# Performance work log

Hardware: AMD Instinct MI355X
Metric: run time of the kernel (lower is better)

The kernel has to match this reference:

```python
import jax, jax.numpy as jnp
import numpy as np

B, K, U = 4096, 512, 3
P, LIFT, HID, NSUB = 5, 32, 128, 10
RATE_LO, RATE_HI = 0.01, 3.0
BASAL_LO, BASAL_HI = 0.0, 0.3


def _xavier(key, shape):
    fan_in, fan_out = shape[1], shape[0]
    lim = np.sqrt(6.0 / (fan_in + fan_out))
    return jax.random.uniform(key, shape, jnp.float32, -lim, lim)


def setup_inputs() -> dict:
    key = jax.random.key(0)
    ks = jax.random.split(key, 10)
    return {
        "y0": jax.random.uniform(ks[0], (B, P), jnp.float32),
        "u_seq": jax.random.uniform(ks[1], (B, K, U), jnp.float32),
        "dt_seq": jax.random.uniform(ks[2], (B, K), jnp.float32),
        # lift: Linear(in_u+P -> LIFT)
        "Wl": _xavier(ks[3], (LIFT, U + P)),
        "bl": jnp.zeros((LIFT,), jnp.float32),
        # GRU (single layer): weight_ih (3H, LIFT), weight_hh (3H, H)
        "W_ih": _xavier(ks[4], (3 * HID, LIFT)),
        "b_ih": jnp.zeros((3 * HID,), jnp.float32),
        "W_hh": _xavier(ks[5], (3 * HID, HID)),
        "b_hh": jnp.zeros((3 * HID,), jnp.float32),
        # head: Linear(H -> 13)
        "Wh": _xavier(ks[6], (13, HID)),
        "bh": jnp.zeros((13,), jnp.float32),
        # bolus-to-state jump matrix (in_u, P)
        "u_to_y_jump": 0.1 * jax.random.uniform(ks[7], (U, P), jnp.float32),
    }


def _rhs(y, theta):
    # y: (B,5) [A,D,G,J,M]; theta: (B,13) [kf1..4, kr1..4, kj1..5]
    A, D, G, J, M = (y[:, i] for i in range(5))
    kf1, kf2, kf3, kf4, kr1, kr2, kr3, kr4, kj1, kj2, kj3, kj4, kj5 = (
        theta[:, i] for i in range(13))
    dA = -kf1 * A + kr1 * D + kj1
    dD = kf1 * A - kr1 * D - kf2 * D + kr2 * G + kj2
    dG = kf2 * D - kr2 * G - kf3 * G + kr3 * J + kj3
    dJ = kf3 * G - kr3 * J - kf4 * J + kr4 * M + kj4
    dM = kf4 * J - kr4 * M + kj5
    return jnp.stack([dA, dD, dG, dJ, dM], axis=-1)


def _rk4(y, h, theta):
    # h: (B,1) substep size
    k1 = _rhs(y, theta)
    k2 = _rhs(y + 0.5 * h * k1, theta)
    k3 = _rhs(y + 0.5 * h * k2, theta)
    k4 = _rhs(y + h * k3, theta)
    return jnp.maximum(y + h / 6.0 * (k1 + 2.0 * k2 + 2.0 * k3 + k4), 0.0)


def reference(y0, u_seq, dt_seq, Wl, bl, W_ih, b_ih, W_hh, b_hh, Wh, bh, u_to_y_jump):
    Bb = y0.shape[0]
    hid = W_hh.shape[1]

    def step(carry, inp):
        y_prev, hst = carry
        u_k, dt_k = inp  # (B,U), (B,)
        feat = jnp.concatenate([u_k, jax.lax.stop_gradient(y_prev)], axis=-1)
        x = jax.nn.silu(feat @ Wl.T + bl)
        # PyTorch GRUCell math
        gx = x @ W_ih.T + b_ih
        gh = hst @ W_hh.T + b_hh
        gxr, gxz, gxn = jnp.split(gx, 3, axis=-1)
        ghr, ghz, ghn = jnp.split(gh, 3, axis=-1)
        r = jax.nn.sigmoid(gxr + ghr)
        zg = jax.nn.sigmoid(gxz + ghz)
        n = jnp.tanh(gxn + r * ghn)
        h_new = (1.0 - zg) * n + zg * hst
        raw = h_new @ Wh.T + bh
        rates = RATE_LO + (RATE_HI - RATE_LO) * jax.nn.sigmoid(raw[:, 0:8])
        basal = BASAL_LO + (BASAL_HI - BASAL_LO) * jax.nn.sigmoid(raw[:, 8:13])
        theta = jnp.concatenate([rates, basal], axis=-1)
        y = y_prev + u_k @ u_to_y_jump
        hsub = (dt_k / float(NSUB))[:, None]
        for _ in range(NSUB):
            y = _rk4(y, hsub, theta)
        return (y, h_new), (y, theta)

    y_init = y0 + 0.01
    h0 = jnp.zeros((Bb, hid), dtype=y0.dtype)
    # scan over time: (K,B,...)
    _, (ys, thetas) = jax.lax.scan(
        step, (y_init, h0), (u_seq.transpose(1, 0, 2), dt_seq.T))
    y_out = ys.transpose(1, 0, 2)        # (B,K,P)
    theta_out = thetas.transpose(1, 0, 2)  # (B,K,13)
    return y_out, theta_out
```

## Files before the change

kernel.cpp:

```cpp
#include <hip/hip_runtime.h>
#include <cstdint>
#include <cstddef>


#define KTOT 512
#define BB   16

typedef _Float16 half8 __attribute__((ext_vector_type(8)));
typedef float    f32x4 __attribute__((ext_vector_type(4)));

struct __align__(16) Smem {
  _Float16 hf16[BB][136];
  float Wlt[8][32];
  float bl[32];
  float brz[256];
  float bnx[128];
  float bnh[128];
  float bhv[16];
  float theta[BB][14];
  float yst[BB][8];
  float ust[2][BB][4];
  float dtst[2][BB];
};

__device__ __forceinline__ float sigm(float x)     { return 1.f / (1.f + __expf(-x)); }
__device__ __forceinline__ float tanhfast(float x) { return 1.f - 2.f / (1.f + __expf(2.f * x)); }

template<int CTRL>
__device__ __forceinline__ float dppf(float x) {
  return __int_as_float(__builtin_amdgcn_mov_dpp(__float_as_int(x), CTRL, 0xf, 0xf, true));
}
#define QP_PLUS  0x39
#define QP_MINUS 0x93
#define QB0 0x00
#define QB1 0x55
#define QB2 0xAA
#define QB3 0xFF

#define MATMUL(Yr, Y4r, Xr, X4r, ALPHA) do {                                  \
  float xm_[5], xp_[5];                                                       \
  _Pragma("unroll")                                                           \
  for (int j_ = 0; j_ < 5; j_++) {                                            \
    xm_[j_] = dppf<QP_MINUS>(Xr[j_]);                                         \
    xp_[j_] = dppf<QP_PLUS >(Xr[j_]);                                         \
  }                                                                           \
  _Pragma("unroll")                                                           \
  for (int j_ = 0; j_ < 5; j_++) {                                            \
    const float ac_ = Zl*xm_[j_] + Zd*Xr[j_] + Zu*xp_[j_] + Zu4*X4r[j_];      \
    const float a4_ = Z43*Xr[j_] + Z44*X4r[j_];                               \
    Yr[j_]  = ((j_ == s_) ? 1.f : 0.f) + (ALPHA)*ac_;                         \
    Y4r[j_] = ((j_ == 4 ) ? 1.f : 0.f) + (ALPHA)*a4_;                         \
  } } while (0)

__global__ __launch_bounds__(256, 1) void rnn_scan_kernel(
    const float* __restrict__ y0,    const float* __restrict__ u_seq,
    const float* __restrict__ dt_sq, const float* __restrict__ Wl,
    const float* __restrict__ bl,    const float* __restrict__ W_ih,
    const float* __restrict__ b_ih,  const float* __restrict__ W_hh,
    const float* __restrict__ b_hh,  const float* __restrict__ Wh,
    const float* __restrict__ bh,    const float* __restrict__ jmp,
    float* __restrict__ y_out, float* __restrict__ th_out)
{
  __shared__ Smem sm;
  const int t   = threadIdx.x;
  const int w   = t >> 6;
  const int l   = t & 63;
  const int n16 = l & 15;
  const int q   = l >> 4;
  const int B0  = blockIdx.x * BB;

  for (int i = t; i < 32*8; i += 256) { const int oo = i >> 3, c = i & 7;
    sm.Wlt[c][oo] = Wl[i]; }
  if (t < 32)  sm.bl[t] = bl[t];
  sm.brz[t] = b_ih[t] + b_hh[t];
  if (t < 128) { sm.bnx[t] = b_ih[256+t]; sm.bnh[t] = b_hh[256+t]; }
  if (t < 16)  sm.bhv[t] = (t < 13) ? bh[t] : 0.f;
  if (t < 128) { const int b = t >> 3, i = t & 7;
    sm.yst[b][i] = (i < 5) ? (y0[(size_t)(B0+b)*5 + i] + 0.01f) : 0.f; }
  if (t < 48) { const int b = t/3, c = t - b*3;
    sm.ust[0][b][c] = u_seq[((size_t)(B0+b)*KTOT + 0)*3 + c]; }
  if (t >= 48 && t < 64) sm.dtst[0][t-48] = dt_sq[(size_t)(B0+(t-48))*KTOT + 0];

  half8 whf[4];
  #pragma unroll
  for (int ks = 0; ks < 4; ks++)
    #pragma unroll
    for (int i = 0; i < 8; i++) {
      const int kk = ks*32 + q*8 + i;
      whf[ks][i] = (n16 < 13) ? (_Float16)Wh[n16*128 + kk] : (_Float16)0.f;
    }

  half8 wihR[2], wihZ[2], wihN[2], whhR[2][4], whhZ[2][4], whhN[2][4];
  #pragma unroll
  for (int p = 0; p < 2; p++) {
    const int jR = (2*w + p)*16 + n16;
    const int jZ = jR + 128, jN = jR + 256;
    #pragma unroll
    for (int i = 0; i < 8; i++) {
      const int kk = q*8 + i;
      wihR[p][i] = (_Float16)W_ih[jR*32 + kk];
      wihZ[p][i] = (_Float16)W_ih[jZ*32 + kk];
      wihN[p][i] = (_Float16)W_ih[jN*32 + kk];
    }
    #pragma unroll
    for (int ks = 0; ks < 4; ks++)
      #pragma unroll
      for (int i = 0; i < 8; i++) {
        const int kk = ks*32 + q*8 + i;
        whhR[p][ks][i] = (_Float16)W_hh[jR*128 + kk];
        whhZ[p][ks][i] = (_Float16)W_hh[jZ*128 + kk];
        whhN[p][ks][i] = (_Float16)W_hh[jN*128 + kk];
      }
  }

  float hreg[2][4];
  #pragma unroll
  for (int p = 0; p < 2; p++)
    #pragma unroll
    for (int rg = 0; rg < 4; rg++) hreg[p][rg] = 0.f;
  half8 hfrag[4];
  #pragma unroll
  for (int ks = 0; ks < 4; ks++)
    #pragma unroll
    for (int i = 0; i < 8; i++) hfrag[ks][i] = (_Float16)0.f;

  const int s_ = l & 3, b4 = l >> 2;
  const float jr0 = jmp[0*5 + s_], jr1 = jmp[1*5 + s_], jr2 = jmp[2*5 + s_];
  const float j40 = (s_==3) ? jmp[4]  : 0.f;
  const float j41 = (s_==3) ? jmp[9]  : 0.f;
  const float j42 = (s_==3) ? jmp[14] : 0.f;

  const int yb = t/5, yi = t - yb*5;
  float* yo_base = y_out + ((size_t)(B0 + (yb & 15))*KTOT)*5 + yi;
  const int ts = (t >= 48) ? (t - 48) : 0;
  const int tb = ts/13, tn = ts - tb*13;
  float* th_base = th_out + ((size_t)(B0 + tb)*KTOT)*13 + tn;
  const int upb = l/3, upc = l - upb*3;

  __syncthreads();

  const f32x4 zero4 = {0.f, 0.f, 0.f, 0.f};

  #pragma unroll 1
  for (int k = 0; k < KTOT; k++) {
    const int buf  = k & 1;
    const int nbuf = (k + 1) & 1;
    const int kp   = (k + 1 < KTOT) ? (k + 1) : (KTOT - 1);

    float pref_u = 0.f, pref_dt = 0.f;
    if (w == 1 && l < 48)
      pref_u = u_seq[((size_t)(B0 + upb)*KTOT + kp)*3 + upc];
    if (w == 2 && l < 16)
      pref_dt = dt_sq[(size_t)(B0 + l)*KTOT + kp];
    if (k > 0) {
      if (t < 80)  yo_base[(size_t)(k-1)*5]  = sm.yst[yb][yi];
      if (t >= 48) th_base[(size_t)(k-1)*13] = sm.theta[tb][tn];
    }
    const float u0 = sm.ust[buf][n16][0], u1 = sm.ust[buf][n16][1], u2 = sm.ust[buf][n16][2];
    const float ya = sm.yst[n16][0], yB = sm.yst[n16][1], yc = sm.yst[n16][2],
                yd = sm.yst[n16][3], ye = sm.yst[n16][4];
    half8 xf;
    #pragma unroll
    for (int i = 0; i < 8; i++) {
      const int oo = q*8 + i;
      const float a = sm.bl[oo]
        + u0*sm.Wlt[0][oo] + u1*sm.Wlt[1][oo] + u2*sm.Wlt[2][oo]
        + ya*sm.Wlt[3][oo] + yB*sm.Wlt[4][oo] + yc*sm.Wlt[5][oo]
        + yd*sm.Wlt[6][oo] + ye*sm.Wlt[7][oo];
      xf[i] = (_Float16)(a * sigm(a));
    }
    f32x4 accR[2], accZ[2], accXN[2], accHN[2];
    #pragma unroll
    for (int p = 0; p < 2; p++) {
      accR[p]  = __builtin_amdgcn_mfma_f32_16x16x32_f16(xf, wihR[p], zero4, 0,0,0);
      accZ[p]  = __builtin_amdgcn_mfma_f32_16x16x32_f16(xf, wihZ[p], zero4, 0,0,0);
      accXN[p] = __builtin_amdgcn_mfma_f32_16x16x32_f16(xf, wihN[p], zero4, 0,0,0);
      accHN[p] = zero4;
      #pragma unroll
      for (int ks = 0; ks < 4; ks++) {
        accR[p]  = __builtin_amdgcn_mfma_f32_16x16x32_f16(hfrag[ks], whhR[p][ks], accR[p], 0,0,0);
        accZ[p]  = __builtin_amdgcn_mfma_f32_16x16x32_f16(hfrag[ks], whhZ[p][ks], accZ[p], 0,0,0);
        accHN[p] = __builtin_amdgcn_mfma_f32_16x16x32_f16(hfrag[ks], whhN[p][ks], accHN[p], 0,0,0);
      }
    }
    #pragma unroll
    for (int p = 0; p < 2; p++) {
      const int jl = 32*w + 16*p + n16;
      const float br = sm.brz[jl], bz = sm.brz[128 + jl];
      const float bx = sm.bnx[jl], bn = sm.bnh[jl];
      #pragma unroll
      for (int rg = 0; rg < 4; rg++) {
        const float r  = sigm(accR[p][rg] + br);
        const float z  = sigm(accZ[p][rg] + bz);
        const float nn = tanhfast(accXN[p][rg] + bx + r*(accHN[p][rg] + bn));
        const float ho = hreg[p][rg];
        const float hn = nn + z*(ho - nn);
        hreg[p][rg] = hn;
        sm.hf16[q*4 + rg][jl] = (_Float16)hn;
      }
    }
    if (w == 1 && l < 48) sm.ust[nbuf][upb][upc] = pref_u;
    if (w == 2 && l < 16) sm.dtst[nbuf][l] = pref_dt;
    __syncthreads();

    #pragma unroll
    for (int ks = 0; ks < 4; ks++)
      hfrag[ks] = *(const half8*)&sm.hf16[n16][ks*32 + q*8];

    if (w == 0) {
      f32x4 accH = zero4;
      #pragma unroll
      for (int ks = 0; ks < 4; ks++)
        accH = __builtin_amdgcn_mfma_f32_16x16x32_f16(hfrag[ks], whf[ks], accH, 0,0,0);
      const float bb_ = sm.bhv[n16];
      #pragma unroll
      for (int rg = 0; rg < 4; rg++) {
        const float sg  = sigm(accH[rg] + bb_);
        const float thv = (n16 < 8) ? (0.01f + 2.99f*sg) : (0.3f*sg);
        if (n16 < 13) sm.theta[q*4 + rg][n16] = thv;
      }
      const float* th = sm.theta[b4];
      const float dt = sm.dtst[buf][b4];
      const float h  = dt * 0.1f;
      const float thm = th[s_ ? (s_ - 1) : 0];
      const float Zl  = s_ ? h*thm : 0.f;
      const float krs = s_ ? th[3 + s_] : 0.f;
      const float Zd  = -h*(th[s_] + krs);
      const float Zur = h*th[4 + s_];
      const float Zu  = (s_ < 3) ? Zur : 0.f;
      const float Zu4 = (s_ == 3) ? Zur : 0.f;
      const float Z43 = h*th[3];
      const float Z44 = -h*th[7];
      const float c0 = th[8], c1 = th[9], c2 = th[10], c3 = th[11], c4 = th[12];
      float Xa[5], Xa4[5], Xb[5], Xb4[5];
      #pragma unroll
      for (int j = 0; j < 5; j++) {
        const float zr = (j == s_) ? Zd : ((j == s_ + 1) ? Zur : ((j + 1 == s_) ? Zl : 0.f));
        Xa[j] = ((j == s_) ? 1.f : 0.f) + 0.25f*zr;
      }
      Xa4[0] = 0.f; Xa4[1] = 0.f; Xa4[2] = 0.f;
      Xa4[3] = 0.25f*Z43; Xa4[4] = 1.f + 0.25f*Z44;
      MATMUL(Xb, Xb4, Xa, Xa4, (1.f/3.f));
      MATMUL(Xa, Xa4, Xb, Xb4, 0.5f);
      const float bv  = h*(Xa[0]*c0 + Xa[1]*c1 + Xa[2]*c2 + Xa[3]*c3 + Xa[4]*c4);
      const float bv4 = h*(Xa4[0]*c0 + Xa4[1]*c1 + Xa4[2]*c2 + Xa4[3]*c3 + Xa4[4]*c4);
      MATMUL(Xb, Xb4, Xa, Xa4, 1.f);
      const float uu0 = sm.ust[buf][b4][0], uu1 = sm.ust[buf][b4][1], uu2 = sm.ust[buf][b4][2];
      float y  = sm.yst[b4][s_] + uu0*jr0 + uu1*jr1 + uu2*jr2;
      float y4 = sm.yst[b4][4]  + uu0*j40 + uu1*j41 + uu2*j42;
      #pragma unroll
      for (int ss = 0; ss < 10; ss++) {
        const float v0 = dppf<QB0>(y), v1 = dppf<QB1>(y),
                    v2 = dppf<QB2>(y), v3 = dppf<QB3>(y);
        const float v4 = dppf<QB3>(y4);
        const float yn  = fmaxf(bv  + Xb[0]*v0 + Xb[1]*v1 + Xb[2]*v2 + Xb[3]*v3 + Xb[4]*v4, 0.f);
        const float y4n = fmaxf(bv4 + Xb4[0]*v0 + Xb4[1]*v1 + Xb4[2]*v2 + Xb4[3]*v3 + Xb4[4]*v4, 0.f);
        y = yn; y4 = y4n;
      }
      sm.yst[b4][s_] = y;
      if (s_ == 3) sm.yst[b4][4] = y4;
    }
    __syncthreads();
  }

  if (t < 80)  yo_base[(size_t)(KTOT-1)*5]  = sm.yst[yb][yi];
  if (t >= 48) th_base[(size_t)(KTOT-1)*13] = sm.theta[tb][tn];
}

extern "C" void kernel_launch(void* const* d_in, const int* in_sizes, int n_in,
                              void* d_out, int out_size, void* d_ws, size_t ws_size,
                              hipStream_t stream) {
  const float* y0     = (const float*)d_in[0];
  const float* u_seq  = (const float*)d_in[1];
  const float* dt_sq  = (const float*)d_in[2];
  const float* Wl     = (const float*)d_in[3];
  const float* bl     = (const float*)d_in[4];
  const float* W_ih   = (const float*)d_in[5];
  const float* b_ih   = (const float*)d_in[6];
  const float* W_hh   = (const float*)d_in[7];
  const float* b_hh   = (const float*)d_in[8];
  const float* Wh     = (const float*)d_in[9];
  const float* bh     = (const float*)d_in[10];
  const float* jmp    = (const float*)d_in[11];
  float* y_out  = (float*)d_out;
  float* th_out = y_out + (size_t)4096 * KTOT * 5;
  rnn_scan_kernel<<<256, 256, 0, stream>>>(
      y0, u_seq, dt_sq, Wl, bl, W_ih, b_ih, W_hh, b_hh, Wh, bh, jmp, y_out, th_out);
}
```

Baseline: 1.687 ms.

## Split GRU gates across 8 waves and precompute hidden matmul ahead of lift

```diff
diff --git a/kernel.cpp b/kernel.cpp
--- a/kernel.cpp
+++ b/kernel.cpp
@@ -11,8 +11,7 @@
 
 struct __align__(16) Smem {
   _Float16 hf16[BB][136];
-  float Wlt[8][32];
-  float bl[32];
+  _Float16 xls[BB][32];
   float brz[256];
   float bnx[128];
   float bnh[128];
@@ -52,7 +51,7 @@
     Y4r[j_] = ((j_ == 4 ) ? 1.f : 0.f) + (ALPHA)*a4_;                         \
   } } while (0)
 
-__global__ __launch_bounds__(256, 1) void rnn_scan_kernel(
+__global__ __launch_bounds__(512, 2) void rnn_scan_kernel(
     const float* __restrict__ y0,    const float* __restrict__ u_seq,
     const float* __restrict__ dt_sq, const float* __restrict__ Wl,
     const float* __restrict__ bl,    const float* __restrict__ W_ih,
@@ -69,17 +68,21 @@
   const int q   = l >> 4;
   const int B0  = blockIdx.x * BB;
 
-  for (int i = t; i < 32*8; i += 256) { const int oo = i >> 3, c = i & 7;
-    sm.Wlt[c][oo] = Wl[i]; }
-  if (t < 32)  sm.bl[t] = bl[t];
-  sm.brz[t] = b_ih[t] + b_hh[t];
+  if (t < 256) sm.brz[t] = b_ih[t] + b_hh[t];
   if (t < 128) { sm.bnx[t] = b_ih[256+t]; sm.bnh[t] = b_hh[256+t]; }
   if (t < 16)  sm.bhv[t] = (t < 13) ? bh[t] : 0.f;
-  if (t < 128) { const int b = t >> 3, i = t & 7;
+  if (t >= 256 && t < 384) { const int b = (t-256) >> 3, i = (t-256) & 7;
     sm.yst[b][i] = (i < 5) ? (y0[(size_t)(B0+b)*5 + i] + 0.01f) : 0.f; }
-  if (t < 48) { const int b = t/3, c = t - b*3;
+  if (t >= 384 && t < 432) { const int b = (t-384)/3, c = (t-384) - ((t-384)/3)*3;
     sm.ust[0][b][c] = u_seq[((size_t)(B0+b)*KTOT + 0)*3 + c]; }
-  if (t >= 48 && t < 64) sm.dtst[0][t-48] = dt_sq[(size_t)(B0+(t-48))*KTOT + 0];
+  if (t >= 432 && t < 448) sm.dtst[0][t-432] = dt_sq[(size_t)(B0+(t-432))*KTOT + 0];
+
+  const int lb = t >> 5;
+  const int lo = t & 31;
+  float wlc[8];
+  #pragma unroll
+  for (int c = 0; c < 8; c++) wlc[c] = Wl[lo*8 + c];
+  const float blv = bl[lo];
 
   half8 whf[4];
   #pragma unroll
@@ -90,39 +93,29 @@
       whf[ks][i] = (n16 < 13) ? (_Float16)Wh[n16*128 + kk] : (_Float16)0.f;
     }
 
-  half8 wihR[2], wihZ[2], wihN[2], whhR[2][4], whhZ[2][4], whhN[2][4];
-  #pragma unroll
-  for (int p = 0; p < 2; p++) {
-    const int jR = (2*w + p)*16 + n16;
-    const int jZ = jR + 128, jN = jR + 256;
+  const int jR = w*16 + n16;
+  const int jZ = jR + 128, jN = jR + 256;
+  half8 wihR, wihZ, wihN, whhR[4], whhZ[4], whhN[4];
+  #pragma unroll
+  for (int i = 0; i < 8; i++) {
+    const int kk = q*8 + i;
+    wihR[i] = (_Float16)W_ih[jR*32 + kk];
+    wihZ[i] = (_Float16)W_ih[jZ*32 + kk];
+    wihN[i] = (_Float16)W_ih[jN*32 + kk];
+  }
+  #pragma unroll
+  for (int ks = 0; ks < 4; ks++)
     #pragma unroll
     for (int i = 0; i < 8; i++) {
-      const int kk = q*8 + i;
-      wihR[p][i] = (_Float16)W_ih[jR*32 + kk];
-      wihZ[p][i] = (_Float16)W_ih[jZ*32 + kk];
-      wihN[p][i] = (_Float16)W_ih[jN*32 + kk];
-    }
-    #pragma unroll
-    for (int ks = 0; ks < 4; ks++)
-      #pragma unroll
-      for (int i = 0; i < 8; i++) {
-        const int kk = ks*32 + q*8 + i;
-        whhR[p][ks][i] = (_Float16)W_hh[jR*128 + kk];
-        whhZ[p][ks][i] = (_Float16)W_hh[jZ*128 + kk];
-        whhN[p][ks][i] = (_Float16)W_hh[jN*128 + kk];
-      }
-  }
-
-  float hreg[2][4];
-  #pragma unroll
-  for (int p = 0; p < 2; p++)
-    #pragma unroll
-    for (int rg = 0; rg < 4; rg++) hreg[p][rg] = 0.f;
-  half8 hfrag[4];
-  #pragma unroll
-  for (int ks = 0; ks < 4; ks++)
-    #pragma unroll
-    for (int i = 0; i < 8; i++) hfrag[ks][i] = (_Float16)0.f;
+      const int kk = ks*32 + q*8 + i;
+      whhR[ks][i] = (_Float16)W_hh[jR*128 + kk];
+      whhZ[ks][i] = (_Float16)W_hh[jZ*128 + kk];
+      whhN[ks][i] = (_Float16)W_hh[jN*128 + kk];
+    }
+
+  float hreg[4] = {0.f, 0.f, 0.f, 0.f};
+  const f32x4 zero4 = {0.f, 0.f, 0.f, 0.f};
+  f32x4 accPreR = zero4, accPreZ = zero4, accPreN = zero4;
 
   const int s_ = l & 3, b4 = l >> 2;
   const float jr0 = jmp[0*5 + s_], jr1 = jmp[1*5 + s_], jr2 = jmp[2*5 + s_];
@@ -130,16 +123,20 @@
   const float j41 = (s_==3) ? jmp[9]  : 0.f;
   const float j42 = (s_==3) ? jmp[14] : 0.f;
 
-  const int yb = t/5, yi = t - yb*5;
+  const int yb = t/5, yi = t - (t/5)*5;
   float* yo_base = y_out + ((size_t)(B0 + (yb & 15))*KTOT)*5 + yi;
-  const int ts = (t >= 48) ? (t - 48) : 0;
-  const int tb = ts/13, tn = ts - tb*13;
-  float* th_base = th_out + ((size_t)(B0 + tb)*KTOT)*13 + tn;
-  const int upb = l/3, upc = l - upb*3;
+  const int ts = (t >= 80) ? (t - 80) : 0;
+  const int tb = ts/13, tn = ts - (ts/13)*13;
+  float* th_base = th_out + ((size_t)(B0 + (tb & 15))*KTOT)*13 + tn;
+  const int upb = l/3, upc = l - (l/3)*3;
 
   __syncthreads();
 
-  const f32x4 zero4 = {0.f, 0.f, 0.f, 0.f};
+  const float br  = sm.brz[jR];
+  const float bz  = sm.brz[128 + jR];
+  const float bx  = sm.bnx[jR];
+  const float bn  = sm.bnh[jR];
+  const float bb_ = sm.bhv[n16];
 
   #pragma unroll 1
   for (int k = 0; k < KTOT; k++) {
@@ -147,72 +144,64 @@
     const int nbuf = (k + 1) & 1;
     const int kp   = (k + 1 < KTOT) ? (k + 1) : (KTOT - 1);
 
+    {
+      const f32x4 uu = *(const f32x4*)&sm.ust[buf][lb][0];
+      const f32x4 ya = *(const f32x4*)&sm.yst[lb][0];
+      const f32x4 yc = *(const f32x4*)&sm.yst[lb][4];
+      const float a = blv
+        + uu[0]*wlc[0] + uu[1]*wlc[1] + uu[2]*wlc[2]
+        + ya[0]*wlc[3] + ya[1]*wlc[4] + ya[2]*wlc[5] + ya[3]*wlc[6]
+        + yc[0]*wlc[7];
+      sm.xls[lb][lo] = (_Float16)(a * sigm(a));
+    }
+    __syncthreads();
+
+    if (k > 0) {
+      if (t < 80)        yo_base[(size_t)(k-1)*5]  = sm.yst[yb][yi];
+      else if (t < 288)  th_base[(size_t)(k-1)*13] = sm.theta[tb][tn];
+    }
+    {
+      const half8 xf = *(const half8*)&sm.xls[n16][q*8];
+      const f32x4 accR  = __builtin_amdgcn_mfma_f32_16x16x32_f16(xf, wihR, accPreR, 0,0,0);
+      const f32x4 accZ  = __builtin_amdgcn_mfma_f32_16x16x32_f16(xf, wihZ, accPreZ, 0,0,0);
+      const f32x4 accXN = __builtin_amdgcn_mfma_f32_16x16x32_f16(xf, wihN, zero4,   0,0,0);
+      #pragma unroll
+      for (int rg = 0; rg < 4; rg++) {
+        const float r  = sigm(accR[rg] + br);
+        const float z  = sigm(accZ[rg] + bz);
+        const float nn = tanhfast(accXN[rg] + bx + r*(accPreN[rg] + bn));
+        const float ho = hreg[rg];
+        const float hn = nn + z*(ho - nn);
+        hreg[rg] = hn;
+        sm.hf16[q*4 + rg][jR] = (_Float16)hn;
+      }
+    }
+    __syncthreads();
+
     float pref_u = 0.f, pref_dt = 0.f;
     if (w == 1 && l < 48)
       pref_u = u_seq[((size_t)(B0 + upb)*KTOT + kp)*3 + upc];
     if (w == 2 && l < 16)
       pref_dt = dt_sq[(size_t)(B0 + l)*KTOT + kp];
-    if (k > 0) {
-      if (t < 80)  yo_base[(size_t)(k-1)*5]  = sm.yst[yb][yi];
-      if (t >= 48) th_base[(size_t)(k-1)*13] = sm.theta[tb][tn];
-    }
-    const float u0 = sm.ust[buf][n16][0], u1 = sm.ust[buf][n16][1], u2 = sm.ust[buf][n16][2];
-    const float ya = sm.yst[n16][0], yB = sm.yst[n16][1], yc = sm.yst[n16][2],
-                yd = sm.yst[n16][3], ye = sm.yst[n16][4];
-    half8 xf;
-    #pragma unroll
-    for (int i = 0; i < 8; i++) {
-      const int oo = q*8 + i;
-      const float a = sm.bl[oo]
-        + u0*sm.Wlt[0][oo] + u1*sm.Wlt[1][oo] + u2*sm.Wlt[2][oo]
-        + ya*sm.Wlt[3][oo] + yB*sm.Wlt[4][oo] + yc*sm.Wlt[5][oo]
-        + yd*sm.Wlt[6][oo] + ye*sm.Wlt[7][oo];
-      xf[i] = (_Float16)(a * sigm(a));
-    }
-    f32x4 accR[2], accZ[2], accXN[2], accHN[2];
-    #pragma unroll
-    for (int p = 0; p < 2; p++) {
-      accR[p]  = __builtin_amdgcn_mfma_f32_16x16x32_f16(xf, wihR[p], zero4, 0,0,0);
-      accZ[p]  = __builtin_amdgcn_mfma_f32_16x16x32_f16(xf, wihZ[p], zero4, 0,0,0);
-      accXN[p] = __builtin_amdgcn_mfma_f32_16x16x32_f16(xf, wihN[p], zero4, 0,0,0);
-      accHN[p] = zero4;
-      #pragma unroll
-      for (int ks = 0; ks < 4; ks++) {
-        accR[p]  = __builtin_amdgcn_mfma_f32_16x16x32_f16(hfrag[ks], whhR[p][ks], accR[p], 0,0,0);
-        accZ[p]  = __builtin_amdgcn_mfma_f32_16x16x32_f16(hfrag[ks], whhZ[p][ks], accZ[p], 0,0,0);
-        accHN[p] = __builtin_amdgcn_mfma_f32_16x16x32_f16(hfrag[ks], whhN[p][ks], accHN[p], 0,0,0);
-      }
-    }
-    #pragma unroll
-    for (int p = 0; p < 2; p++) {
-      const int jl = 32*w + 16*p + n16;
-      const float br = sm.brz[jl], bz = sm.brz[128 + jl];
-      const float bx = sm.bnx[jl], bn = sm.bnh[jl];
-      #pragma unroll
-      for (int rg = 0; rg < 4; rg++) {
-        const float r  = sigm(accR[p][rg] + br);
-        const float z  = sigm(accZ[p][rg] + bz);
-        const float nn = tanhfast(accXN[p][rg] + bx + r*(accHN[p][rg] + bn));
-        const float ho = hreg[p][rg];
-        const float hn = nn + z*(ho - nn);
-        hreg[p][rg] = hn;
-        sm.hf16[q*4 + rg][jl] = (_Float16)hn;
-      }
-    }
-    if (w == 1 && l < 48) sm.ust[nbuf][upb][upc] = pref_u;
-    if (w == 2 && l < 16) sm.dtst[nbuf][l] = pref_dt;
-    __syncthreads();
-
+
+    half8 hfrag[4];
     #pragma unroll
     for (int ks = 0; ks < 4; ks++)
       hfrag[ks] = *(const half8*)&sm.hf16[n16][ks*32 + q*8];
 
+    accPreR = zero4; accPreZ = zero4; accPreN = zero4;
+    #pragma unroll
+    for (int ks = 0; ks < 4; ks++) {
+      accPreR = __builtin_amdgcn_mfma_f32_16x16x32_f16(hfrag[ks], whhR[ks], accPreR, 0,0,0);
+      accPreZ = __builtin_amdgcn_mfma_f32_16x16x32_f16(hfrag[ks], whhZ[ks], accPreZ, 0,0,0);
+      accPreN = __builtin_amdgcn_mfma_f32_16x16x32_f16(hfrag[ks], whhN[ks], accPreN, 0,0,0);
+    }
+
     if (w == 0) {
       f32x4 accH = zero4;
       #pragma unroll
       for (int ks = 0; ks < 4; ks++)
         accH = __builtin_amdgcn_mfma_f32_16x16x32_f16(hfrag[ks], whf[ks], accH, 0,0,0);
-      const float bb_ = sm.bhv[n16];
       #pragma unroll
       for (int rg = 0; rg < 4; rg++) {
         const float sg  = sigm(accH[rg] + bb_);
@@ -260,11 +249,13 @@
       sm.yst[b4][s_] = y;
       if (s_ == 3) sm.yst[b4][4] = y4;
     }
+    if (w == 1 && l < 48) sm.ust[nbuf][upb][upc] = pref_u;
+    if (w == 2 && l < 16) sm.dtst[nbuf][l] = pref_dt;
     __syncthreads();
   }
 
-  if (t < 80)  yo_base[(size_t)(KTOT-1)*5]  = sm.yst[yb][yi];
-  if (t >= 48) th_base[(size_t)(KTOT-1)*13] = sm.theta[tb][tn];
+  if (t < 80)        yo_base[(size_t)(KTOT-1)*5]  = sm.yst[yb][yi];
+  else if (t < 288)  th_base[(size_t)(KTOT-1)*13] = sm.theta[tb][tn];
 }
 
 extern "C" void kernel_launch(void* const* d_in, const int* in_sizes, int n_in,
@@ -284,6 +275,6 @@
   const float* jmp    = (const float*)d_in[11];
   float* y_out  = (float*)d_out;
   float* th_out = y_out + (size_t)4096 * KTOT * 5;
-  rnn_scan_kernel<<<256, 256, 0, stream>>>(
+  rnn_scan_kernel<<<256, 512, 0, stream>>>(
       y0, u_seq, dt_sq, Wl, bl, W_ih, b_ih, W_hh, b_hh, Wh, bh, jmp, y_out, th_out);
 }
```

Result: faster. 1.474 ms (-12.6%).
